# Optimization experiments

Measured on AMD Instinct MI355X. Metric: run time of the kernel, lower is better.

## Reference

```python
import jax, jax.numpy as jnp
import numpy as np

B, S, H = 4, 256, 768
F = 32            # num_features
T = 256           # TAG_HIDDEN_SIZE
WD = 64           # WIDTH_HIDDEN_SIZE
C = 16            # num_tags


def setup_inputs() -> dict:
    key = jax.random.key(0)
    ks = jax.random.split(key, 10)
    inp = {
        "final_hidden": jax.random.normal(ks[0], (B, S, H), jnp.float32),
        "feature_vecs": jax.random.normal(ks[1], (B, S, F), jnp.float32),
        # Linear params stored [in, out] (transposed vs torch; same math)
        "start_W": jax.random.normal(ks[2], (H + F, T), jnp.float32) * (1.0 / np.sqrt(H + F)),
        "start_b": jnp.zeros((T,), jnp.float32),
        "end_W": jax.random.normal(ks[3], (H + F, T), jnp.float32) * (1.0 / np.sqrt(H + F)),
        "end_b": jnp.zeros((T,), jnp.float32),
        "U": jax.random.normal(ks[4], (T, C, T), jnp.float32) * (1.0 / np.sqrt(T)),
        "width_hidden": jax.random.uniform(ks[5], (S, S, WD), jnp.float32),
        "lin_W": jax.random.normal(ks[6], (2 * T + WD, C), jnp.float32) * (1.0 / np.sqrt(2 * T + WD)),
        "lin_b": jnp.zeros((C,), jnp.float32),
    }
    return inp


def reference(final_hidden, feature_vecs, start_W, start_b, end_W, end_b, U, width_hidden, lin_W, lin_b):
    # dropout p=0.0 -> identity
    x = jnp.concatenate([final_hidden, feature_vecs], axis=-1)   # [B,S,H+F]
    s = x @ start_W + start_b                                    # [B,S,T]
    e = x @ end_W + end_b                                        # [B,S,T]

    # biaffine term: einsum('bsh,hci->bsci') then ('bsci,bei->bsec')
    sU = jnp.einsum('bst,tcu->bscu', s, U)                       # [B,S,C,T]
    pre = jnp.einsum('bscu,beu->bsec', sU, e)                    # [B,S,S,C]

    # pairwise FFN, fused: Linear over concat(start, end, width) decomposes
    # into three small matmuls + broadcast adds (same math, no O(S^2*(2T+W)) buffer)
    Ws, We, Ww = lin_W[:T], lin_W[T:2 * T], lin_W[2 * T:]
    ffn = (jnp.einsum('bst,tc->bsc', s, Ws)[:, :, None, :]
           + jnp.einsum('bet,tc->bec', e, We)[:, None, :, :]
           + jnp.einsum('sew,wc->sec', width_hidden, Ww)[None]
           + lin_b)                                              # [B,S,S,C]
    return pre + ffn
```

## Files before the change

### kernel.cpp

```cpp
#include <hip/hip_runtime.h>


#define B_ 4
#define S_ 256
#define H_ 768
#define F_ 32
#define T_ 256
#define C_ 16
#define R_ 1024
#define HF 800
#define HFP 832

typedef unsigned short u16;
typedef __attribute__((ext_vector_type(8))) short short8;
typedef __attribute__((ext_vector_type(4))) float f32x4;

__device__ __forceinline__ u16 f2b(float x) {
    unsigned u = __builtin_bit_cast(unsigned, x);
    u += 0x7FFF + ((u >> 16) & 1);
    return (u16)(u >> 16);
}
__device__ __forceinline__ float b2f(u16 b) {
    unsigned u = ((unsigned)b) << 16;
    return __builtin_bit_cast(float, u);
}

__global__ __launch_bounds__(256)
void k_prep(const float* __restrict__ fh, const float* __restrict__ fv,
            const float* __restrict__ sW, const float* __restrict__ eW,
            const float* __restrict__ U,  const float* __restrict__ WH,
            const float* __restrict__ linW, const float* __restrict__ linb,
            u16* __restrict__ Xb, u16* __restrict__ Wt, u16* __restrict__ Ut,
            float* __restrict__ WC)
{
    const int bid = blockIdx.x;
    const int tid = threadIdx.x;

    if (bid < 832) {
        int idx = bid * 256 + tid;
        int r = idx / 208, c4 = idx % 208;
        int k = c4 * 4;
        float4 v;
        if (k < H_)       v = *(const float4*)&fh[r * H_ + k];
        else if (k < HF)  v = *(const float4*)&fv[r * F_ + k - H_];
        else              v = make_float4(0.f, 0.f, 0.f, 0.f);
        ushort4 o; o.x = f2b(v.x); o.y = f2b(v.y); o.z = f2b(v.z); o.w = f2b(v.w);
        *(ushort4*)&Xb[(size_t)r * HFP + k] = o;
        return;
    }
    if (bid < 1232) {
        __shared__ float t_[32][33];
        int bid2 = bid - 832;
        int k0 = (bid2 / 16) * 32;
        int j0 = (bid2 % 16) * 32;
        const float* src = (j0 < T_) ? sW : eW;
        const int js = (j0 < T_) ? j0 : j0 - T_;
        {
            int jl = tid & 31, kl0 = (tid >> 5) * 4;
#pragma unroll
            for (int i = 0; i < 4; ++i)
                t_[kl0 + i][jl] = src[(k0 + kl0 + i) * T_ + js + jl];
        }
        __syncthreads();
        {
            int kl = tid & 31, jl0 = (tid >> 5) * 4;
#pragma unroll
            for (int i = 0; i < 4; ++i)
                Wt[(size_t)(j0 + jl0 + i) * HFP + k0 + kl] = f2b(t_[kl][jl0 + i]);
        }
        return;
    }
    if (bid < 1248) {
        int idx = (bid - 1232) * 256 + tid;
        int r = idx >> 3, c4 = idx & 7;
        ushort4 z; z.x = z.y = z.z = z.w = 0;
        *(ushort4*)&Wt[(size_t)r * HFP + HF + c4 * 4] = z;
        return;
    }
    if (bid < 2272) {
        __shared__ float t_[32][33];
        int bid2 = bid - 1248;
        int cu0 = (bid2 >> 3) * 32;
        int t0  = (bid2 & 7) * 32;
        {
            int cul = tid & 31, tl0 = (tid >> 5) * 4;
#pragma unroll
            for (int i = 0; i < 4; ++i)
                t_[tl0 + i][cul] = U[(size_t)(t0 + tl0 + i) * 4096 + cu0 + cul];
        }
        __syncthreads();
        {
            int tl = tid & 31, cul0 = (tid >> 5) * 4;
#pragma unroll
            for (int i = 0; i < 4; ++i)
                Ut[(size_t)(cu0 + cul0 + i) * T_ + t0 + tl] = f2b(t_[tl][cul0 + i]);
        }
        return;
    }
    {
        __shared__ float Wl[16][64];
        __shared__ float Wwl[64][16];
        int se0 = (bid - 2272) * 16;
        {
            int sel = tid >> 4, w4 = tid & 15;
            *(float4*)&Wl[sel][w4 * 4] = *(const float4*)&WH[(size_t)(se0 + sel) * 64 + w4 * 4];
        }
        {
            int w = tid >> 2, c4 = tid & 3;
            *(float4*)&Wwl[w][c4 * 4] = *(const float4*)&linW[(512 + w) * 16 + c4 * 4];
        }
        __syncthreads();
        int sel = tid >> 4, c = tid & 15;
        float acc = linb[c];
#pragma unroll
        for (int w = 0; w < 64; ++w)
            acc += Wl[sel][w] * Wwl[w][c];
        WC[(size_t)(se0 + sel) * 16 + c] = acc;
    }
}

template<int K, int LDA, int LDB, int MF, int NF, int UNROLL>
__device__ __forceinline__ void core(const u16* __restrict__ A,
                                     const u16* __restrict__ B,
                                     int lr, int kgl, f32x4 acc[MF][NF])
{
    const u16* ap[MF];
    const u16* bp[NF];
#pragma unroll
    for (int i = 0; i < MF; ++i) ap[i] = A + (size_t)(i * 16 + lr) * LDA + kgl * 8;
#pragma unroll
    for (int j = 0; j < NF; ++j) bp[j] = B + (size_t)(j * 16 + lr) * LDB + kgl * 8;

#pragma unroll UNROLL
    for (int k = 0; k < K; k += 32) {
        short8 a[MF], b[NF];
#pragma unroll
        for (int i = 0; i < MF; ++i) a[i] = *(const short8*)(ap[i] + k);
#pragma unroll
        for (int j = 0; j < NF; ++j) b[j] = *(const short8*)(bp[j] + k);
#pragma unroll
        for (int i = 0; i < MF; ++i)
#pragma unroll
            for (int j = 0; j < NF; ++j)
                acc[i][j] = __builtin_amdgcn_mfma_f32_16x16x32_bf16(a[i], b[j], acc[i][j], 0, 0, 0);
    }
}

__global__ __launch_bounds__(256)
void k_se(const u16* __restrict__ Xb, const u16* __restrict__ Wt,
          const float* __restrict__ sb, const float* __restrict__ eb,
          u16* __restrict__ SEb)
{
    const int tid = threadIdx.x;
    const int l = tid & 63, w = tid >> 6;
    const int wr = w >> 1, wc = w & 1;
    const int lr = l & 15, kgl = l >> 4;
    const int bm = blockIdx.x * 64;
    const int bn = blockIdx.y * 64;
    f32x4 acc[2][2] = {};

    core<HFP, HFP, HFP, 2, 2, 2>(Wt + (size_t)(bm + wr * 32) * HFP,
                                 Xb + (size_t)(bn + wc * 32) * HFP,
                                 lr, kgl, acc);

#pragma unroll
    for (int i = 0; i < 2; ++i) {
        int j0 = bm + wr * 32 + i * 16 + kgl * 4;
        float4 bias = (j0 < T_) ? *(const float4*)&sb[j0]
                                : *(const float4*)&eb[j0 - T_];
#pragma unroll
        for (int jj = 0; jj < 2; ++jj) {
            int r = bn + wc * 32 + jj * 16 + lr;
            ushort4 o;
            o.x = f2b(acc[i][jj][0] + bias.x);
            o.y = f2b(acc[i][jj][1] + bias.y);
            o.z = f2b(acc[i][jj][2] + bias.z);
            o.w = f2b(acc[i][jj][3] + bias.w);
            *(ushort4*)&SEb[(size_t)r * 512 + j0] = o;
        }
    }
}

__global__ __launch_bounds__(256)
void k_su_scec(const u16* __restrict__ SEb, const u16* __restrict__ Ut,
               const float* __restrict__ linW,
               u16* __restrict__ SUb, float* __restrict__ SCEC)
{
    const int bid = blockIdx.x;
    const int tid = threadIdx.x;

    if (bid < 256) {
        const int l = tid & 63, w = tid >> 6;
        const int wr = w >> 1, wc = w & 1;
        const int lr = l & 15, kgl = l >> 4;
        const int bm = (bid & 31) * 128;
        const int bn = (bid >> 5) * 128;
        f32x4 acc[4][4] = {};

        core<T_, T_, 512, 4, 4, 2>(Ut + (size_t)(bm + wr * 64) * T_,
                                   SEb + (size_t)(bn + wc * 64) * 512,
                                   lr, kgl, acc);

#pragma unroll
        for (int i = 0; i < 4; ++i) {
            int cu0 = bm + wr * 64 + i * 16 + kgl * 4;
#pragma unroll
            for (int j = 0; j < 4; ++j) {
                int r = bn + wc * 64 + j * 16 + lr;
                ushort4 o;
                o.x = f2b(acc[i][j][0]); o.y = f2b(acc[i][j][1]);
                o.z = f2b(acc[i][j][2]); o.w = f2b(acc[i][j][3]);
                *(ushort4*)&SUb[(size_t)r * 4096 + cu0] = o;
            }
        }
        return;
    }

    __shared__ float SEl[4][512];
    const int r0 = (bid - 256) * 4;
#pragma unroll
    for (int i = 0; i < 2; ++i) {
        int ch = tid + i * 256;
        int rl = ch >> 7, o4 = (ch & 127) * 4;
        ushort4 v = *(const ushort4*)&SEb[(size_t)(r0 + rl) * 512 + o4];
        SEl[rl][o4 + 0] = b2f(v.x); SEl[rl][o4 + 1] = b2f(v.y);
        SEl[rl][o4 + 2] = b2f(v.z); SEl[rl][o4 + 3] = b2f(v.w);
    }
    __syncthreads();
    const int rl = tid >> 6, tq = (tid >> 4) & 3, c = tid & 15;
    const int t0 = tq * 64;
    float accs = 0.f, acce = 0.f;
#pragma unroll 4
    for (int t = t0; t < t0 + 64; ++t) {
        accs += SEl[rl][t]       * linW[t * 16 + c];
        acce += SEl[rl][256 + t] * linW[(256 + t) * 16 + c];
    }
    accs += __shfl_xor(accs, 16); accs += __shfl_xor(accs, 32);
    acce += __shfl_xor(acce, 16); acce += __shfl_xor(acce, 32);
    if (tq == 0) {
        SCEC[(r0 + rl) * 32 + c]      = accs;
        SCEC[(r0 + rl) * 32 + 16 + c] = acce;
    }
}

__global__ __launch_bounds__(256)
void k_pre(const u16* __restrict__ SEb, const u16* __restrict__ SUb,
           const float* __restrict__ SCEC, const float* __restrict__ WC,
           float* __restrict__ OUT)
{
    const int tid = threadIdx.x;
    const int l = tid & 63, w = tid >> 6;
    const int wr = w >> 1, wc = w & 1;
    const int lr = l & 15, kgl = l >> 4;
    const int bm = blockIdx.x * 128;
    const int bn = blockIdx.y * 128;
    const int b  = blockIdx.z;
    f32x4 acc[4][4] = {};

    const u16* An = SUb + ((size_t)b << 20) + (size_t)(bm + wr * 64) * T_;
    const u16* Be = SEb + (size_t)(b << 8) * 512 + 256 + (size_t)(bn + wc * 64) * 512;

    core<T_, T_, 512, 4, 4, 2>(An, Be, lr, kgl, acc);

    const int c0 = kgl * 4;
    float4 scv[4];
#pragma unroll
    for (int i = 0; i < 4; ++i) {
        int s = (bm + wr * 64 + i * 16) >> 4;
        scv[i] = *(const float4*)&SCEC[((b << 8) + s) * 32 + c0];
    }
#pragma unroll
    for (int j = 0; j < 4; ++j) {
        int e = bn + wc * 64 + j * 16 + lr;
        float4 ecv = *(const float4*)&SCEC[((b << 8) + e) * 32 + 16 + c0];
#pragma unroll
        for (int i = 0; i < 4; ++i) {
            int s = (bm + wr * 64 + i * 16) >> 4;
            float4 wcv = *(const float4*)&WC[(size_t)(s * S_ + e) * 16 + c0];
            float4 o;
            o.x = acc[i][j][0] + scv[i].x + ecv.x + wcv.x;
            o.y = acc[i][j][1] + scv[i].y + ecv.y + wcv.y;
            o.z = acc[i][j][2] + scv[i].z + ecv.z + wcv.z;
            o.w = acc[i][j][3] + scv[i].w + ecv.w + wcv.w;
            *(float4*)&OUT[(((size_t)(b << 8) + s) * S_ + e) * 16 + c0] = o;
        }
    }
}

extern "C" void kernel_launch(void* const* d_in, const int* in_sizes, int n_in,
                              void* d_out, int out_size, void* d_ws, size_t ws_size,
                              hipStream_t stream)
{
    const float* fh   = (const float*)d_in[0];
    const float* fv   = (const float*)d_in[1];
    const float* sW   = (const float*)d_in[2];
    const float* sb   = (const float*)d_in[3];
    const float* eW   = (const float*)d_in[4];
    const float* eb   = (const float*)d_in[5];
    const float* U    = (const float*)d_in[6];
    const float* WH   = (const float*)d_in[7];
    const float* linW = (const float*)d_in[8];
    const float* linb = (const float*)d_in[9];
    float* OUT = (float*)d_out;

    char* p = (char*)d_ws;
    u16* SUb = (u16*)p;      p += (size_t)B_ * 4096 * 256 * 2;
    float* WC = (float*)p;   p += (size_t)S_ * S_ * C_ * 4;
    u16* Ut  = (u16*)p;      p += (size_t)4096 * T_ * 2;
    u16* Xb  = (u16*)p;      p += (size_t)R_ * HFP * 2;
    u16* Wt  = (u16*)p;      p += (size_t)512 * HFP * 2;
    u16* SEb = (u16*)p;      p += (size_t)R_ * 512 * 2;
    float* SCEC = (float*)p; p += (size_t)R_ * 32 * 4;

    k_prep<<<dim3(6368), 256, 0, stream>>>(fh, fv, sW, eW, U, WH, linW, linb,
                                           Xb, Wt, Ut, WC);
    k_se  <<<dim3(8, 16), 256, 0, stream>>>(Xb, Wt, sb, eb, SEb);
    k_su_scec<<<dim3(512), 256, 0, stream>>>(SEb, Ut, linW, SUb, SCEC);
    k_pre <<<dim3(32, 2, 4), 256, 0, stream>>>(SEb, SUb, SCEC, WC, OUT);
}
```

Measured before the change: 61.18 us.

## Fuse four stage kernels into one cooperative persistent kernel with grid syncs

Merges the prep, start/end GEMM, SU/SCEC and final biaffine kernels into a single cooperative kernel of 512 blocks. Grid-wide syncs separate the stages, which removes the launch gaps between them. The final stage is retiled to 64x128 tiles so its 512 jobs map one per block. If the cooperative launch fails, the code falls back to four separate launches. Risks include grid.sync overhead, prep work being serialized through a grid-stride loop over 512 blocks, and occupancy limits from __launch_bounds__(256,2).

```diff
diff --git a/kernel.cpp b/kernel.cpp
--- a/kernel.cpp
+++ b/kernel.cpp
@@ -1,4 +1,7 @@
 #include <hip/hip_runtime.h>
+#include <hip/hip_cooperative_groups.h>
+
+namespace cg = cooperative_groups;
 
 
 #define B_ 4
@@ -25,17 +28,41 @@
     return __builtin_bit_cast(float, u);
 }
 
-__global__ __launch_bounds__(256)
-void k_prep(const float* __restrict__ fh, const float* __restrict__ fv,
-            const float* __restrict__ sW, const float* __restrict__ eW,
-            const float* __restrict__ U,  const float* __restrict__ WH,
-            const float* __restrict__ linW, const float* __restrict__ linb,
-            u16* __restrict__ Xb, u16* __restrict__ Wt, u16* __restrict__ Ut,
-            float* __restrict__ WC)
-{
-    const int bid = blockIdx.x;
-    const int tid = threadIdx.x;
-
+template<int K, int LDA, int LDB, int MF, int NF, int UNROLL>
+__device__ __forceinline__ void core(const u16* __restrict__ A,
+                                     const u16* __restrict__ B,
+                                     int lr, int kgl, f32x4 acc[MF][NF])
+{
+    const u16* ap[MF];
+    const u16* bp[NF];
+#pragma unroll
+    for (int i = 0; i < MF; ++i) ap[i] = A + (size_t)(i * 16 + lr) * LDA + kgl * 8;
+#pragma unroll
+    for (int j = 0; j < NF; ++j) bp[j] = B + (size_t)(j * 16 + lr) * LDB + kgl * 8;
+
+#pragma unroll UNROLL
+    for (int k = 0; k < K; k += 32) {
+        short8 a[MF], b[NF];
+#pragma unroll
+        for (int i = 0; i < MF; ++i) a[i] = *(const short8*)(ap[i] + k);
+#pragma unroll
+        for (int j = 0; j < NF; ++j) b[j] = *(const short8*)(bp[j] + k);
+#pragma unroll
+        for (int i = 0; i < MF; ++i)
+#pragma unroll
+            for (int j = 0; j < NF; ++j)
+                acc[i][j] = __builtin_amdgcn_mfma_f32_16x16x32_bf16(a[i], b[j], acc[i][j], 0, 0, 0);
+    }
+}
+
+__device__ __forceinline__ void prep_job(int bid, int tid,
+    const float* __restrict__ fh, const float* __restrict__ fv,
+    const float* __restrict__ sW, const float* __restrict__ eW,
+    const float* __restrict__ U,  const float* __restrict__ WH,
+    const float* __restrict__ linW, const float* __restrict__ linb,
+    u16* __restrict__ Xb, u16* __restrict__ Wt, u16* __restrict__ Ut,
+    float* __restrict__ WC, float* sh)
+{
     if (bid < 832) {
         int idx = bid * 256 + tid;
         int r = idx / 208, c4 = idx % 208;
@@ -46,10 +73,8 @@
         else              v = make_float4(0.f, 0.f, 0.f, 0.f);
         ushort4 o; o.x = f2b(v.x); o.y = f2b(v.y); o.z = f2b(v.z); o.w = f2b(v.w);
         *(ushort4*)&Xb[(size_t)r * HFP + k] = o;
-        return;
-    }
-    if (bid < 1232) {
-        __shared__ float t_[32][33];
+    } else if (bid < 1232) {
+        float (*t_)[33] = (float(*)[33])sh;
         int bid2 = bid - 832;
         int k0 = (bid2 / 16) * 32;
         int j0 = (bid2 % 16) * 32;
@@ -68,17 +93,14 @@
             for (int i = 0; i < 4; ++i)
                 Wt[(size_t)(j0 + jl0 + i) * HFP + k0 + kl] = f2b(t_[kl][jl0 + i]);
         }
-        return;
-    }
-    if (bid < 1248) {
+        __syncthreads();
+    } else if (bid < 1248) {
         int idx = (bid - 1232) * 256 + tid;
         int r = idx >> 3, c4 = idx & 7;
         ushort4 z; z.x = z.y = z.z = z.w = 0;
         *(ushort4*)&Wt[(size_t)r * HFP + HF + c4 * 4] = z;
-        return;
-    }
-    if (bid < 2272) {
-        __shared__ float t_[32][33];
+    } else if (bid < 2272) {
+        float (*t_)[33] = (float(*)[33])sh;
         int bid2 = bid - 1248;
         int cu0 = (bid2 >> 3) * 32;
         int t0  = (bid2 & 7) * 32;
@@ -95,68 +117,40 @@
             for (int i = 0; i < 4; ++i)
                 Ut[(size_t)(cu0 + cul0 + i) * T_ + t0 + tl] = f2b(t_[tl][cul0 + i]);
         }
-        return;
-    }
-    {
-        __shared__ float Wl[16][64];
-        __shared__ float Wwl[64][16];
+        __syncthreads();
+    } else {
+        float* Wl  = sh;
+        float* Wwl = sh + 1024;
         int se0 = (bid - 2272) * 16;
         {
             int sel = tid >> 4, w4 = tid & 15;
-            *(float4*)&Wl[sel][w4 * 4] = *(const float4*)&WH[(size_t)(se0 + sel) * 64 + w4 * 4];
+            *(float4*)&Wl[sel * 64 + w4 * 4] = *(const float4*)&WH[(size_t)(se0 + sel) * 64 + w4 * 4];
         }
         {
             int w = tid >> 2, c4 = tid & 3;
-            *(float4*)&Wwl[w][c4 * 4] = *(const float4*)&linW[(512 + w) * 16 + c4 * 4];
+            *(float4*)&Wwl[w * 16 + c4 * 4] = *(const float4*)&linW[(512 + w) * 16 + c4 * 4];
         }
         __syncthreads();
         int sel = tid >> 4, c = tid & 15;
         float acc = linb[c];
 #pragma unroll
         for (int w = 0; w < 64; ++w)
-            acc += Wl[sel][w] * Wwl[w][c];
+            acc += Wl[sel * 64 + w] * Wwl[w * 16 + c];
         WC[(size_t)(se0 + sel) * 16 + c] = acc;
-    }
-}
-
-template<int K, int LDA, int LDB, int MF, int NF, int UNROLL>
-__device__ __forceinline__ void core(const u16* __restrict__ A,
-                                     const u16* __restrict__ B,
-                                     int lr, int kgl, f32x4 acc[MF][NF])
-{
-    const u16* ap[MF];
-    const u16* bp[NF];
-#pragma unroll
-    for (int i = 0; i < MF; ++i) ap[i] = A + (size_t)(i * 16 + lr) * LDA + kgl * 8;
-#pragma unroll
-    for (int j = 0; j < NF; ++j) bp[j] = B + (size_t)(j * 16 + lr) * LDB + kgl * 8;
-
-#pragma unroll UNROLL
-    for (int k = 0; k < K; k += 32) {
-        short8 a[MF], b[NF];
-#pragma unroll
-        for (int i = 0; i < MF; ++i) a[i] = *(const short8*)(ap[i] + k);
-#pragma unroll
-        for (int j = 0; j < NF; ++j) b[j] = *(const short8*)(bp[j] + k);
-#pragma unroll
-        for (int i = 0; i < MF; ++i)
-#pragma unroll
-            for (int j = 0; j < NF; ++j)
-                acc[i][j] = __builtin_amdgcn_mfma_f32_16x16x32_bf16(a[i], b[j], acc[i][j], 0, 0, 0);
-    }
-}
-
-__global__ __launch_bounds__(256)
-void k_se(const u16* __restrict__ Xb, const u16* __restrict__ Wt,
-          const float* __restrict__ sb, const float* __restrict__ eb,
-          u16* __restrict__ SEb)
-{
-    const int tid = threadIdx.x;
+        __syncthreads();
+    }
+}
+
+__device__ __forceinline__ void se_job(int job, int tid,
+    const u16* __restrict__ Xb, const u16* __restrict__ Wt,
+    const float* __restrict__ sb, const float* __restrict__ eb,
+    u16* __restrict__ SEb)
+{
     const int l = tid & 63, w = tid >> 6;
     const int wr = w >> 1, wc = w & 1;
     const int lr = l & 15, kgl = l >> 4;
-    const int bm = blockIdx.x * 64;
-    const int bn = blockIdx.y * 64;
+    const int bm = (job & 7) * 64;
+    const int bn = (job >> 3) * 64;
     f32x4 acc[2][2] = {};
 
     core<HFP, HFP, HFP, 2, 2, 2>(Wt + (size_t)(bm + wr * 32) * HFP,
@@ -181,50 +175,48 @@
     }
 }
 
-__global__ __launch_bounds__(256)
-void k_su_scec(const u16* __restrict__ SEb, const u16* __restrict__ Ut,
-               const float* __restrict__ linW,
-               u16* __restrict__ SUb, float* __restrict__ SCEC)
-{
-    const int bid = blockIdx.x;
-    const int tid = threadIdx.x;
-
-    if (bid < 256) {
-        const int l = tid & 63, w = tid >> 6;
-        const int wr = w >> 1, wc = w & 1;
-        const int lr = l & 15, kgl = l >> 4;
-        const int bm = (bid & 31) * 128;
-        const int bn = (bid >> 5) * 128;
-        f32x4 acc[4][4] = {};
-
-        core<T_, T_, 512, 4, 4, 2>(Ut + (size_t)(bm + wr * 64) * T_,
-                                   SEb + (size_t)(bn + wc * 64) * 512,
-                                   lr, kgl, acc);
-
-#pragma unroll
-        for (int i = 0; i < 4; ++i) {
-            int cu0 = bm + wr * 64 + i * 16 + kgl * 4;
-#pragma unroll
-            for (int j = 0; j < 4; ++j) {
-                int r = bn + wc * 64 + j * 16 + lr;
-                ushort4 o;
-                o.x = f2b(acc[i][j][0]); o.y = f2b(acc[i][j][1]);
-                o.z = f2b(acc[i][j][2]); o.w = f2b(acc[i][j][3]);
-                *(ushort4*)&SUb[(size_t)r * 4096 + cu0] = o;
-            }
-        }
-        return;
-    }
-
-    __shared__ float SEl[4][512];
-    const int r0 = (bid - 256) * 4;
+__device__ __forceinline__ void su_job(int bid, int tid,
+    const u16* __restrict__ SEb, const u16* __restrict__ Ut,
+    u16* __restrict__ SUb)
+{
+    const int l = tid & 63, w = tid >> 6;
+    const int wr = w >> 1, wc = w & 1;
+    const int lr = l & 15, kgl = l >> 4;
+    const int bm = (bid & 31) * 128;
+    const int bn = (bid >> 5) * 128;
+    f32x4 acc[4][4] = {};
+
+    core<T_, T_, 512, 4, 4, 2>(Ut + (size_t)(bm + wr * 64) * T_,
+                               SEb + (size_t)(bn + wc * 64) * 512,
+                               lr, kgl, acc);
+
+#pragma unroll
+    for (int i = 0; i < 4; ++i) {
+        int cu0 = bm + wr * 64 + i * 16 + kgl * 4;
+#pragma unroll
+        for (int j = 0; j < 4; ++j) {
+            int r = bn + wc * 64 + j * 16 + lr;
+            ushort4 o;
+            o.x = f2b(acc[i][j][0]); o.y = f2b(acc[i][j][1]);
+            o.z = f2b(acc[i][j][2]); o.w = f2b(acc[i][j][3]);
+            *(ushort4*)&SUb[(size_t)r * 4096 + cu0] = o;
+        }
+    }
+}
+
+__device__ __forceinline__ void scec_job(int job, int tid,
+    const u16* __restrict__ SEb, const float* __restrict__ linW,
+    float* __restrict__ SCEC, float* sh)
+{
+    float* SEl = sh;
+    const int r0 = job * 4;
 #pragma unroll
     for (int i = 0; i < 2; ++i) {
         int ch = tid + i * 256;
         int rl = ch >> 7, o4 = (ch & 127) * 4;
         ushort4 v = *(const ushort4*)&SEb[(size_t)(r0 + rl) * 512 + o4];
-        SEl[rl][o4 + 0] = b2f(v.x); SEl[rl][o4 + 1] = b2f(v.y);
-        SEl[rl][o4 + 2] = b2f(v.z); SEl[rl][o4 + 3] = b2f(v.w);
+        SEl[rl * 512 + o4 + 0] = b2f(v.x); SEl[rl * 512 + o4 + 1] = b2f(v.y);
+        SEl[rl * 512 + o4 + 2] = b2f(v.z); SEl[rl * 512 + o4 + 3] = b2f(v.w);
     }
     __syncthreads();
     const int rl = tid >> 6, tq = (tid >> 4) & 3, c = tid & 15;
@@ -232,8 +224,8 @@
     float accs = 0.f, acce = 0.f;
 #pragma unroll 4
     for (int t = t0; t < t0 + 64; ++t) {
-        accs += SEl[rl][t]       * linW[t * 16 + c];
-        acce += SEl[rl][256 + t] * linW[(256 + t) * 16 + c];
+        accs += SEl[rl * 512 + t]       * linW[t * 16 + c];
+        acce += SEl[rl * 512 + 256 + t] * linW[(256 + t) * 16 + c];
     }
     accs += __shfl_xor(accs, 16); accs += __shfl_xor(accs, 32);
     acce += __shfl_xor(acce, 16); acce += __shfl_xor(acce, 32);
@@ -241,50 +233,101 @@
         SCEC[(r0 + rl) * 32 + c]      = accs;
         SCEC[(r0 + rl) * 32 + 16 + c] = acce;
     }
-}
-
-__global__ __launch_bounds__(256)
-void k_pre(const u16* __restrict__ SEb, const u16* __restrict__ SUb,
-           const float* __restrict__ SCEC, const float* __restrict__ WC,
-           float* __restrict__ OUT)
-{
-    const int tid = threadIdx.x;
+    __syncthreads();
+}
+
+__device__ __forceinline__ void pre_job(int bid, int tid,
+    const u16* __restrict__ SEb, const u16* __restrict__ SUb,
+    const float* __restrict__ SCEC, const float* __restrict__ WC,
+    float* __restrict__ OUT)
+{
+    const int b  = bid >> 7;
+    const int q2 = bid & 127;
+    const int bm = (q2 & 63) * 64;
+    const int bn = (q2 >> 6) * 128;
     const int l = tid & 63, w = tid >> 6;
-    const int wr = w >> 1, wc = w & 1;
+    const int wn = w >> 1, we = w & 1;
     const int lr = l & 15, kgl = l >> 4;
-    const int bm = blockIdx.x * 128;
-    const int bn = blockIdx.y * 128;
-    const int b  = blockIdx.z;
-    f32x4 acc[4][4] = {};
-
-    const u16* An = SUb + ((size_t)b << 20) + (size_t)(bm + wr * 64) * T_;
-    const u16* Be = SEb + (size_t)(b << 8) * 512 + 256 + (size_t)(bn + wc * 64) * 512;
-
-    core<T_, T_, 512, 4, 4, 2>(An, Be, lr, kgl, acc);
+    f32x4 acc[2][4] = {};
+
+    const u16* An = SUb + ((size_t)b << 20) + (size_t)(bm + wn * 32) * T_;
+    const u16* Be = SEb + (size_t)(b << 8) * 512 + 256 + (size_t)(bn + we * 64) * 512;
+
+    core<T_, T_, 512, 2, 4, 2>(An, Be, lr, kgl, acc);
 
     const int c0 = kgl * 4;
-    float4 scv[4];
-#pragma unroll
-    for (int i = 0; i < 4; ++i) {
-        int s = (bm + wr * 64 + i * 16) >> 4;
-        scv[i] = *(const float4*)&SCEC[((b << 8) + s) * 32 + c0];
-    }
-#pragma unroll
-    for (int j = 0; j < 4; ++j) {
-        int e = bn + wc * 64 + j * 16 + lr;
-        float4 ecv = *(const float4*)&SCEC[((b << 8) + e) * 32 + 16 + c0];
-#pragma unroll
-        for (int i = 0; i < 4; ++i) {
-            int s = (bm + wr * 64 + i * 16) >> 4;
+#pragma unroll
+    for (int i = 0; i < 2; ++i) {
+        int n0 = bm + wn * 32 + i * 16;
+        int s = n0 >> 4;
+        float4 scv = *(const float4*)&SCEC[((b << 8) + s) * 32 + c0];
+#pragma unroll
+        for (int j = 0; j < 4; ++j) {
+            int e = bn + we * 64 + j * 16 + lr;
+            float4 ecv = *(const float4*)&SCEC[((b << 8) + e) * 32 + 16 + c0];
             float4 wcv = *(const float4*)&WC[(size_t)(s * S_ + e) * 16 + c0];
             float4 o;
-            o.x = acc[i][j][0] + scv[i].x + ecv.x + wcv.x;
-            o.y = acc[i][j][1] + scv[i].y + ecv.y + wcv.y;
-            o.z = acc[i][j][2] + scv[i].z + ecv.z + wcv.z;
-            o.w = acc[i][j][3] + scv[i].w + ecv.w + wcv.w;
+            o.x = acc[i][j][0] + scv.x + ecv.x + wcv.x;
+            o.y = acc[i][j][1] + scv.y + ecv.y + wcv.y;
+            o.z = acc[i][j][2] + scv.z + ecv.z + wcv.z;
+            o.w = acc[i][j][3] + scv.w + ecv.w + wcv.w;
             *(float4*)&OUT[(((size_t)(b << 8) + s) * S_ + e) * 16 + c0] = o;
         }
     }
+}
+
+__global__ __launch_bounds__(256, 2)
+void k_all(const float* fh, const float* fv, const float* sW, const float* sb,
+           const float* eW, const float* eb, const float* U, const float* WH,
+           const float* linW, const float* linb,
+           u16* Xb, u16* Wt, u16* Ut, float* WC, u16* SEb, float* SCEC,
+           u16* SUb, float* OUT)
+{
+    __shared__ float sh[2112];
+    cg::grid_group grid = cg::this_grid();
+    const int nb  = gridDim.x;
+    const int bid = blockIdx.x;
+    const int tid = threadIdx.x;
+
+    for (int job = bid; job < 6368; job += nb)
+        prep_job(job, tid, fh, fv, sW, eW, U, WH, linW, linb, Xb, Wt, Ut, WC, sh);
+    grid.sync();
+
+    if (bid < 128)
+        se_job(bid, tid, Xb, Wt, sb, eb, SEb);
+    grid.sync();
+
+    if (bid < 256) su_job(bid, tid, SEb, Ut, SUb);
+    else           scec_job(bid - 256, tid, SEb, linW, SCEC, sh);
+    grid.sync();
+
+    pre_job(bid, tid, SEb, SUb, SCEC, WC, OUT);
+}
+
+__global__ __launch_bounds__(256)
+void k_prep_sa(const float* fh, const float* fv, const float* sW, const float* eW,
+               const float* U, const float* WH, const float* linW, const float* linb,
+               u16* Xb, u16* Wt, u16* Ut, float* WC)
+{
+    __shared__ float sh[2112];
+    prep_job(blockIdx.x, threadIdx.x, fh, fv, sW, eW, U, WH, linW, linb, Xb, Wt, Ut, WC, sh);
+}
+__global__ __launch_bounds__(256)
+void k_se_sa(const u16* Xb, const u16* Wt, const float* sb, const float* eb, u16* SEb)
+{
+    se_job(blockIdx.x, threadIdx.x, Xb, Wt, sb, eb, SEb);
+}
+__global__ __launch_bounds__(256)
+void k_suscec_sa(const u16* SEb, const u16* Ut, const float* linW, u16* SUb, float* SCEC)
+{
+    __shared__ float sh[2112];
+    if (blockIdx.x < 256) su_job(blockIdx.x, threadIdx.x, SEb, Ut, SUb);
+    else                  scec_job(blockIdx.x - 256, threadIdx.x, SEb, linW, SCEC, sh);
+}
+__global__ __launch_bounds__(256)
+void k_pre_sa(const u16* SEb, const u16* SUb, const float* SCEC, const float* WC, float* OUT)
+{
+    pre_job(blockIdx.x, threadIdx.x, SEb, SUb, SCEC, WC, OUT);
 }
 
 extern "C" void kernel_launch(void* const* d_in, const int* in_sizes, int n_in,
@@ -312,9 +355,18 @@
     u16* SEb = (u16*)p;      p += (size_t)R_ * 512 * 2;
     float* SCEC = (float*)p; p += (size_t)R_ * 32 * 4;
 
-    k_prep<<<dim3(6368), 256, 0, stream>>>(fh, fv, sW, eW, U, WH, linW, linb,
-                                           Xb, Wt, Ut, WC);
-    k_se  <<<dim3(8, 16), 256, 0, stream>>>(Xb, Wt, sb, eb, SEb);
-    k_su_scec<<<dim3(512), 256, 0, stream>>>(SEb, Ut, linW, SUb, SCEC);
-    k_pre <<<dim3(32, 2, 4), 256, 0, stream>>>(SEb, SUb, SCEC, WC, OUT);
-}
+    void* args[] = {(void*)&fh, (void*)&fv, (void*)&sW, (void*)&sb, (void*)&eW,
+                    (void*)&eb, (void*)&U,  (void*)&WH, (void*)&linW, (void*)&linb,
+                    (void*)&Xb, (void*)&Wt, (void*)&Ut, (void*)&WC, (void*)&SEb,
+                    (void*)&SCEC, (void*)&SUb, (void*)&OUT};
+    hipError_t err = hipLaunchCooperativeKernel((const void*)k_all, dim3(512), dim3(256),
+                                                args, 0, stream);
+    if (err != hipSuccess) {
+        (void)hipGetLastError();
+        k_prep_sa<<<dim3(6368), 256, 0, stream>>>(fh, fv, sW, eW, U, WH, linW, linb,
+                                                  Xb, Wt, Ut, WC);
+        k_se_sa<<<dim3(128), 256, 0, stream>>>(Xb, Wt, sb, eb, SEb);
+        k_suscec_sa<<<dim3(512), 256, 0, stream>>>(SEb, Ut, linW, SUb, SCEC);
+        k_pre_sa<<<dim3(512), 256, 0, stream>>>(SEb, SUb, SCEC, WC, OUT);
+    }
+}
```

Result: slower. 236.5 us (+286.5%).

## Rebalance work across kernels and shrink GEMM tiles for more blocks

Applied to the files above, without the earlier changes.

The prep work is redistributed across the pipeline. The U transpose/convert now runs alongside the start/end GEMM, and the width-hidden projection (WC) runs alongside the SU GEMM and SCEC blocks, so the first kernel is shorter. The SE, SU and final biaffine GEMMs use smaller per-block tiles, which gives 256, 512 and 512 blocks to fill more CUs on the MI355X. The trade-off is less operand reuse per block and mixed heterogeneous blocks inside each launch.

```diff
diff --git a/kernel.cpp b/kernel.cpp
--- a/kernel.cpp
+++ b/kernel.cpp
@@ -25,13 +25,37 @@
     return __builtin_bit_cast(float, u);
 }
 
+template<int K, int LDA, int LDB, int MF, int NF, int UNROLL>
+__device__ __forceinline__ void core(const u16* __restrict__ A,
+                                     const u16* __restrict__ B,
+                                     int lr, int kgl, f32x4 acc[MF][NF])
+{
+    const u16* ap[MF];
+    const u16* bp[NF];
+#pragma unroll
+    for (int i = 0; i < MF; ++i) ap[i] = A + (size_t)(i * 16 + lr) * LDA + kgl * 8;
+#pragma unroll
+    for (int j = 0; j < NF; ++j) bp[j] = B + (size_t)(j * 16 + lr) * LDB + kgl * 8;
+
+#pragma unroll UNROLL
+    for (int k = 0; k < K; k += 32) {
+        short8 a[MF], b[NF];
+#pragma unroll
+        for (int i = 0; i < MF; ++i) a[i] = *(const short8*)(ap[i] + k);
+#pragma unroll
+        for (int j = 0; j < NF; ++j) b[j] = *(const short8*)(bp[j] + k);
+#pragma unroll
+        for (int i = 0; i < MF; ++i)
+#pragma unroll
+            for (int j = 0; j < NF; ++j)
+                acc[i][j] = __builtin_amdgcn_mfma_f32_16x16x32_bf16(a[i], b[j], acc[i][j], 0, 0, 0);
+    }
+}
+
 __global__ __launch_bounds__(256)
-void k_prep(const float* __restrict__ fh, const float* __restrict__ fv,
+void k_cvt1(const float* __restrict__ fh, const float* __restrict__ fv,
             const float* __restrict__ sW, const float* __restrict__ eW,
-            const float* __restrict__ U,  const float* __restrict__ WH,
-            const float* __restrict__ linW, const float* __restrict__ linb,
-            u16* __restrict__ Xb, u16* __restrict__ Wt, u16* __restrict__ Ut,
-            float* __restrict__ WC)
+            u16* __restrict__ Xb, u16* __restrict__ Wt)
 {
     const int bid = blockIdx.x;
     const int tid = threadIdx.x;
@@ -46,9 +70,7 @@
         else              v = make_float4(0.f, 0.f, 0.f, 0.f);
         ushort4 o; o.x = f2b(v.x); o.y = f2b(v.y); o.z = f2b(v.z); o.w = f2b(v.w);
         *(ushort4*)&Xb[(size_t)r * HFP + k] = o;
-        return;
-    }
-    if (bid < 1232) {
+    } else if (bid < 1232) {
         __shared__ float t_[32][33];
         int bid2 = bid - 832;
         int k0 = (bid2 / 16) * 32;
@@ -68,18 +90,53 @@
             for (int i = 0; i < 4; ++i)
                 Wt[(size_t)(j0 + jl0 + i) * HFP + k0 + kl] = f2b(t_[kl][jl0 + i]);
         }
-        return;
-    }
-    if (bid < 1248) {
+    } else {
         int idx = (bid - 1232) * 256 + tid;
         int r = idx >> 3, c4 = idx & 7;
         ushort4 z; z.x = z.y = z.z = z.w = 0;
         *(ushort4*)&Wt[(size_t)r * HFP + HF + c4 * 4] = z;
+    }
+}
+
+__global__ __launch_bounds__(256)
+void k_se_cvtu(const u16* __restrict__ Xb, const u16* __restrict__ Wt,
+               const float* __restrict__ sb, const float* __restrict__ eb,
+               const float* __restrict__ U,
+               u16* __restrict__ SEb, u16* __restrict__ Ut)
+{
+    const int bid = blockIdx.x;
+    const int tid = threadIdx.x;
+
+    if (bid < 256) {
+        const int l = tid & 63, w = tid >> 6;
+        const int wj = w & 1, wr2 = w >> 1;
+        const int lr = l & 15, kgl = l >> 4;
+        const int bm = (bid & 15) * 32;
+        const int bn = (bid >> 4) * 64;
+        f32x4 acc[1][2] = {};
+
+        core<HFP, HFP, HFP, 1, 2, 2>(Wt + (size_t)(bm + wj * 16) * HFP,
+                                     Xb + (size_t)(bn + wr2 * 32) * HFP,
+                                     lr, kgl, acc);
+
+        int j0 = bm + wj * 16 + kgl * 4;
+        float4 bias = (j0 < T_) ? *(const float4*)&sb[j0]
+                                : *(const float4*)&eb[j0 - T_];
+#pragma unroll
+        for (int jj = 0; jj < 2; ++jj) {
+            int r = bn + wr2 * 32 + jj * 16 + lr;
+            ushort4 o;
+            o.x = f2b(acc[0][jj][0] + bias.x);
+            o.y = f2b(acc[0][jj][1] + bias.y);
+            o.z = f2b(acc[0][jj][2] + bias.z);
+            o.w = f2b(acc[0][jj][3] + bias.w);
+            *(ushort4*)&SEb[(size_t)r * 512 + j0] = o;
+        }
         return;
     }
-    if (bid < 2272) {
+    {
         __shared__ float t_[32][33];
-        int bid2 = bid - 1248;
+        int bid2 = bid - 256;
         int cu0 = (bid2 >> 3) * 32;
         int t0  = (bid2 & 7) * 32;
         {
@@ -95,118 +152,37 @@
             for (int i = 0; i < 4; ++i)
                 Ut[(size_t)(cu0 + cul0 + i) * T_ + t0 + tl] = f2b(t_[tl][cul0 + i]);
         }
-        return;
-    }
-    {
-        __shared__ float Wl[16][64];
-        __shared__ float Wwl[64][16];
-        int se0 = (bid - 2272) * 16;
-        {
-            int sel = tid >> 4, w4 = tid & 15;
-            *(float4*)&Wl[sel][w4 * 4] = *(const float4*)&WH[(size_t)(se0 + sel) * 64 + w4 * 4];
-        }
-        {
-            int w = tid >> 2, c4 = tid & 3;
-            *(float4*)&Wwl[w][c4 * 4] = *(const float4*)&linW[(512 + w) * 16 + c4 * 4];
-        }
-        __syncthreads();
-        int sel = tid >> 4, c = tid & 15;
-        float acc = linb[c];
-#pragma unroll
-        for (int w = 0; w < 64; ++w)
-            acc += Wl[sel][w] * Wwl[w][c];
-        WC[(size_t)(se0 + sel) * 16 + c] = acc;
-    }
-}
-
-template<int K, int LDA, int LDB, int MF, int NF, int UNROLL>
-__device__ __forceinline__ void core(const u16* __restrict__ A,
-                                     const u16* __restrict__ B,
-                                     int lr, int kgl, f32x4 acc[MF][NF])
-{
-    const u16* ap[MF];
-    const u16* bp[NF];
-#pragma unroll
-    for (int i = 0; i < MF; ++i) ap[i] = A + (size_t)(i * 16 + lr) * LDA + kgl * 8;
-#pragma unroll
-    for (int j = 0; j < NF; ++j) bp[j] = B + (size_t)(j * 16 + lr) * LDB + kgl * 8;
-
-#pragma unroll UNROLL
-    for (int k = 0; k < K; k += 32) {
-        short8 a[MF], b[NF];
-#pragma unroll
-        for (int i = 0; i < MF; ++i) a[i] = *(const short8*)(ap[i] + k);
-#pragma unroll
-        for (int j = 0; j < NF; ++j) b[j] = *(const short8*)(bp[j] + k);
-#pragma unroll
-        for (int i = 0; i < MF; ++i)
-#pragma unroll
-            for (int j = 0; j < NF; ++j)
-                acc[i][j] = __builtin_amdgcn_mfma_f32_16x16x32_bf16(a[i], b[j], acc[i][j], 0, 0, 0);
     }
 }
 
 __global__ __launch_bounds__(256)
-void k_se(const u16* __restrict__ Xb, const u16* __restrict__ Wt,
-          const float* __restrict__ sb, const float* __restrict__ eb,
-          u16* __restrict__ SEb)
-{
-    const int tid = threadIdx.x;
-    const int l = tid & 63, w = tid >> 6;
-    const int wr = w >> 1, wc = w & 1;
-    const int lr = l & 15, kgl = l >> 4;
-    const int bm = blockIdx.x * 64;
-    const int bn = blockIdx.y * 64;
-    f32x4 acc[2][2] = {};
-
-    core<HFP, HFP, HFP, 2, 2, 2>(Wt + (size_t)(bm + wr * 32) * HFP,
-                                 Xb + (size_t)(bn + wc * 32) * HFP,
-                                 lr, kgl, acc);
-
-#pragma unroll
-    for (int i = 0; i < 2; ++i) {
-        int j0 = bm + wr * 32 + i * 16 + kgl * 4;
-        float4 bias = (j0 < T_) ? *(const float4*)&sb[j0]
-                                : *(const float4*)&eb[j0 - T_];
-#pragma unroll
-        for (int jj = 0; jj < 2; ++jj) {
-            int r = bn + wc * 32 + jj * 16 + lr;
-            ushort4 o;
-            o.x = f2b(acc[i][jj][0] + bias.x);
-            o.y = f2b(acc[i][jj][1] + bias.y);
-            o.z = f2b(acc[i][jj][2] + bias.z);
-            o.w = f2b(acc[i][jj][3] + bias.w);
-            *(ushort4*)&SEb[(size_t)r * 512 + j0] = o;
-        }
-    }
-}
-
-__global__ __launch_bounds__(256)
-void k_su_scec(const u16* __restrict__ SEb, const u16* __restrict__ Ut,
-               const float* __restrict__ linW,
-               u16* __restrict__ SUb, float* __restrict__ SCEC)
+void k_su_scec_wc(const u16* __restrict__ SEb, const u16* __restrict__ Ut,
+                  const float* __restrict__ linW, const float* __restrict__ linb,
+                  const float* __restrict__ WH,
+                  u16* __restrict__ SUb, float* __restrict__ SCEC,
+                  float* __restrict__ WC)
 {
     const int bid = blockIdx.x;
     const int tid = threadIdx.x;
 
-    if (bid < 256) {
+    if (bid < 512) {
         const int l = tid & 63, w = tid >> 6;
-        const int wr = w >> 1, wc = w & 1;
+        const int wcu = w & 1, wr2 = w >> 1;
         const int lr = l & 15, kgl = l >> 4;
         const int bm = (bid & 31) * 128;
-        const int bn = (bid >> 5) * 128;
-        f32x4 acc[4][4] = {};
-
-        core<T_, T_, 512, 4, 4, 2>(Ut + (size_t)(bm + wr * 64) * T_,
-                                   SEb + (size_t)(bn + wc * 64) * 512,
+        const int bn = (bid >> 5) * 64;
+        f32x4 acc[4][2] = {};
+
+        core<T_, T_, 512, 4, 2, 2>(Ut + (size_t)(bm + wcu * 64) * T_,
+                                   SEb + (size_t)(bn + wr2 * 32) * 512,
                                    lr, kgl, acc);
 
 #pragma unroll
         for (int i = 0; i < 4; ++i) {
-            int cu0 = bm + wr * 64 + i * 16 + kgl * 4;
-#pragma unroll
-            for (int j = 0; j < 4; ++j) {
-                int r = bn + wc * 64 + j * 16 + lr;
+            int cu0 = bm + wcu * 64 + i * 16 + kgl * 4;
+#pragma unroll
+            for (int j = 0; j < 2; ++j) {
+                int r = bn + wr2 * 32 + j * 16 + lr;
                 ushort4 o;
                 o.x = f2b(acc[i][j][0]); o.y = f2b(acc[i][j][1]);
                 o.z = f2b(acc[i][j][2]); o.w = f2b(acc[i][j][3]);
@@ -215,31 +191,59 @@
         }
         return;
     }
-
-    __shared__ float SEl[4][512];
-    const int r0 = (bid - 256) * 4;
-#pragma unroll
-    for (int i = 0; i < 2; ++i) {
-        int ch = tid + i * 256;
-        int rl = ch >> 7, o4 = (ch & 127) * 4;
-        ushort4 v = *(const ushort4*)&SEb[(size_t)(r0 + rl) * 512 + o4];
-        SEl[rl][o4 + 0] = b2f(v.x); SEl[rl][o4 + 1] = b2f(v.y);
-        SEl[rl][o4 + 2] = b2f(v.z); SEl[rl][o4 + 3] = b2f(v.w);
-    }
-    __syncthreads();
-    const int rl = tid >> 6, tq = (tid >> 4) & 3, c = tid & 15;
-    const int t0 = tq * 64;
-    float accs = 0.f, acce = 0.f;
+    if (bid < 768) {
+        __shared__ float SEl[4][512];
+        const int r0 = (bid - 512) * 4;
+#pragma unroll
+        for (int i = 0; i < 2; ++i) {
+            int ch = tid + i * 256;
+            int rl = ch >> 7, o4 = (ch & 127) * 4;
+            ushort4 v = *(const ushort4*)&SEb[(size_t)(r0 + rl) * 512 + o4];
+            SEl[rl][o4 + 0] = b2f(v.x); SEl[rl][o4 + 1] = b2f(v.y);
+            SEl[rl][o4 + 2] = b2f(v.z); SEl[rl][o4 + 3] = b2f(v.w);
+        }
+        __syncthreads();
+        const int rl = tid >> 6, tq = (tid >> 4) & 3, c = tid & 15;
+        const int t0 = tq * 64;
+        float accs = 0.f, acce = 0.f;
 #pragma unroll 4
-    for (int t = t0; t < t0 + 64; ++t) {
-        accs += SEl[rl][t]       * linW[t * 16 + c];
-        acce += SEl[rl][256 + t] * linW[(256 + t) * 16 + c];
-    }
-    accs += __shfl_xor(accs, 16); accs += __shfl_xor(accs, 32);
-    acce += __shfl_xor(acce, 16); acce += __shfl_xor(acce, 32);
-    if (tq == 0) {
-        SCEC[(r0 + rl) * 32 + c]      = accs;
-        SCEC[(r0 + rl) * 32 + 16 + c] = acce;
+        for (int t = t0; t < t0 + 64; ++t) {
+            accs += SEl[rl][t]       * linW[t * 16 + c];
+            acce += SEl[rl][256 + t] * linW[(256 + t) * 16 + c];
+        }
+        accs += __shfl_xor(accs, 16); accs += __shfl_xor(accs, 32);
+        acce += __shfl_xor(acce, 16); acce += __shfl_xor(acce, 32);
+        if (tq == 0) {
+            SCEC[(r0 + rl) * 32 + c]      = accs;
+            SCEC[(r0 + rl) * 32 + 16 + c] = acce;
+        }
+        return;
+    }
+    {
+        __shared__ float Wl[16][64];
+        __shared__ float Wwl[64][16];
+        const int se0 = (bid - 768) * 128;
+        {
+            int w0 = tid >> 2, c4 = tid & 3;
+            *(float4*)&Wwl[w0][c4 * 4] = *(const float4*)&linW[(512 + w0) * 16 + c4 * 4];
+        }
+        const int sel = tid >> 4, c = tid & 15;
+        const float lb = linb[c];
+#pragma unroll
+        for (int it = 0; it < 8; ++it) {
+            __syncthreads();
+            {
+                int w4 = tid & 15;
+                *(float4*)&Wl[sel][w4 * 4] =
+                    *(const float4*)&WH[(size_t)(se0 + it * 16 + sel) * 64 + w4 * 4];
+            }
+            __syncthreads();
+            float acc = lb;
+#pragma unroll
+            for (int w0 = 0; w0 < 64; ++w0)
+                acc += Wl[sel][w0] * Wwl[w0][c];
+            WC[(size_t)(se0 + it * 16 + sel) * 16 + c] = acc;
+        }
     }
 }
 
@@ -248,40 +252,38 @@
            const float* __restrict__ SCEC, const float* __restrict__ WC,
            float* __restrict__ OUT)
 {
+    const int bid = blockIdx.x;
     const int tid = threadIdx.x;
+    const int b  = bid >> 7;
+    const int q2 = bid & 127;
+    const int bm = (q2 & 63) * 64;
+    const int bn = (q2 >> 6) * 128;
     const int l = tid & 63, w = tid >> 6;
-    const int wr = w >> 1, wc = w & 1;
+    const int wn = w >> 1, we = w & 1;
     const int lr = l & 15, kgl = l >> 4;
-    const int bm = blockIdx.x * 128;
-    const int bn = blockIdx.y * 128;
-    const int b  = blockIdx.z;
-    f32x4 acc[4][4] = {};
-
-    const u16* An = SUb + ((size_t)b << 20) + (size_t)(bm + wr * 64) * T_;
-    const u16* Be = SEb + (size_t)(b << 8) * 512 + 256 + (size_t)(bn + wc * 64) * 512;
-
-    core<T_, T_, 512, 4, 4, 2>(An, Be, lr, kgl, acc);
+    f32x4 acc[2][4] = {};
+
+    const u16* An = SUb + ((size_t)b << 20) + (size_t)(bm + wn * 32) * T_;
+    const u16* Be = SEb + (size_t)(b << 8) * 512 + 256 + (size_t)(bn + we * 64) * 512;
+
+    core<T_, T_, 512, 2, 4, 2>(An, Be, lr, kgl, acc);
 
     const int c0 = kgl * 4;
-    float4 scv[4];
-#pragma unroll
-    for (int i = 0; i < 4; ++i) {
-        int s = (bm + wr * 64 + i * 16) >> 4;
-        scv[i] = *(const float4*)&SCEC[((b << 8) + s) * 32 + c0];
-    }
-#pragma unroll
-    for (int j = 0; j < 4; ++j) {
-        int e = bn + wc * 64 + j * 16 + lr;
-        float4 ecv = *(const float4*)&SCEC[((b << 8) + e) * 32 + 16 + c0];
-#pragma unroll
-        for (int i = 0; i < 4; ++i) {
-            int s = (bm + wr * 64 + i * 16) >> 4;
+#pragma unroll
+    for (int i = 0; i < 2; ++i) {
+        int n0 = bm + wn * 32 + i * 16;
+        int s = n0 >> 4;
+        float4 scv = *(const float4*)&SCEC[((b << 8) + s) * 32 + c0];
+#pragma unroll
+        for (int j = 0; j < 4; ++j) {
+            int e = bn + we * 64 + j * 16 + lr;
+            float4 ecv = *(const float4*)&SCEC[((b << 8) + e) * 32 + 16 + c0];
             float4 wcv = *(const float4*)&WC[(size_t)(s * S_ + e) * 16 + c0];
             float4 o;
-            o.x = acc[i][j][0] + scv[i].x + ecv.x + wcv.x;
-            o.y = acc[i][j][1] + scv[i].y + ecv.y + wcv.y;
-            o.z = acc[i][j][2] + scv[i].z + ecv.z + wcv.z;
-            o.w = acc[i][j][3] + scv[i].w + ecv.w + wcv.w;
+            o.x = acc[i][j][0] + scv.x + ecv.x + wcv.x;
+            o.y = acc[i][j][1] + scv.y + ecv.y + wcv.y;
+            o.z = acc[i][j][2] + scv.z + ecv.z + wcv.z;
+            o.w = acc[i][j][3] + scv.w + ecv.w + wcv.w;
             *(float4*)&OUT[(((size_t)(b << 8) + s) * S_ + e) * 16 + c0] = o;
         }
     }
@@ -312,9 +314,9 @@
     u16* SEb = (u16*)p;      p += (size_t)R_ * 512 * 2;
     float* SCEC = (float*)p; p += (size_t)R_ * 32 * 4;
 
-    k_prep<<<dim3(6368), 256, 0, stream>>>(fh, fv, sW, eW, U, WH, linW, linb,
-                                           Xb, Wt, Ut, WC);
-    k_se  <<<dim3(8, 16), 256, 0, stream>>>(Xb, Wt, sb, eb, SEb);
-    k_su_scec<<<dim3(512), 256, 0, stream>>>(SEb, Ut, linW, SUb, SCEC);
-    k_pre <<<dim3(32, 2, 4), 256, 0, stream>>>(SEb, SUb, SCEC, WC, OUT);
-}
+    k_cvt1<<<dim3(1248), 256, 0, stream>>>(fh, fv, sW, eW, Xb, Wt);
+    k_se_cvtu<<<dim3(1280), 256, 0, stream>>>(Xb, Wt, sb, eb, U, SEb, Ut);
+    k_su_scec_wc<<<dim3(1280), 256, 0, stream>>>(SEb, Ut, linW, linb, WH,
+                                                 SUb, SCEC, WC);
+    k_pre<<<dim3(512), 256, 0, stream>>>(SEb, SUb, SCEC, WC, OUT);
+}
```

Result: slower. 64.27 us (+5.0%).
